# Performance work log

Hardware: AMD Instinct MI355X
Metric: run time of the kernel (lower is better)

Reference implementation:

```python
import jax, jax.numpy as jnp
import numpy as np

B, F, L, H, D = 8, 256, 1024, 4, 256   # batch, filters, seq_len, n_head(=dilation), d_qkv
MODEL = H * F                          # = H * D = 1024
WIN = 128                              # local_window_size


def _local_mask():
    m = np.ones((L, L), dtype=bool)
    m = np.tril(m, WIN - 1)
    m = np.triu(m, -(WIN - 1))
    return jnp.asarray(m)


def setup_inputs() -> dict:
    key = jax.random.key(0)
    ks = jax.random.split(key, 12)
    s = lambda n: 1.0 / np.sqrt(n)
    xav = np.sqrt(6.0 / (L + L))
    return {
        "x": jax.random.normal(ks[0], (B, F, L, H), jnp.float32),
        "Wq_w": jax.random.normal(ks[1], (D, F), jnp.float32) * s(F),
        "Wq_b": jnp.zeros((D,), jnp.float32),
        "Wk_w": jax.random.normal(ks[2], (D, F), jnp.float32) * s(F),
        "Wk_b": jnp.zeros((D,), jnp.float32),
        "Wv_w": jax.random.normal(ks[3], (D, F), jnp.float32) * s(F),
        "Wv_b": jnp.zeros((D,), jnp.float32),
        "w_bias": jax.random.uniform(ks[4], (L, L), jnp.float32, -xav, xav),
        "out_w": jax.random.normal(ks[5], (H * D, MODEL), jnp.float32) * s(H * D),
        "out_b": jnp.zeros((MODEL,), jnp.float32),
        "ln_g": jnp.ones((MODEL,), jnp.float32),
        "ln_b": jnp.zeros((MODEL,), jnp.float32),
        "local_mask": _local_mask(),
    }


def _flatten(y):
    # N C L H -> N L (H C): H outer, C inner in the flattened dim
    n = y.shape[0]
    return y.transpose(0, 2, 3, 1).reshape(n, L, -1)


def reference(x, Wq_w, Wq_b, Wk_w, Wk_b, Wv_w, Wv_b, w_bias, out_w, out_b, ln_g, ln_b, local_mask):
    def proj(w, b):
        # 1x1 Conv2d over (L,H) == channel matmul
        y = jnp.einsum('nclh,dc->ndlh', x, w) + b[None, :, None, None]
        return _flatten(y)

    q = proj(Wq_w, Wq_b)   # [B, L, H*D]
    k = proj(Wk_w, Wk_b)
    v = proj(Wv_w, Wv_b)

    wb = w_bias * local_mask.astype(w_bias.dtype)  # masked bias (masked entries -> 0, exp -> 1)
    ew = jnp.exp(wb)                                # [L, L]
    ek = jnp.exp(k)                                 # [B, L, H*D]
    num = jnp.einsum('ts,nsd->ntd', ew, ek * v)
    den = jnp.einsum('ts,nsd->ntd', ew, ek)
    y = jax.nn.sigmoid(q) * num / den               # [B, L, H*D]

    h = y @ out_w + out_b + _flatten(x)             # residual with flattened input
    mu = jnp.mean(h, axis=-1, keepdims=True)
    var = jnp.mean(jnp.square(h - mu), axis=-1, keepdims=True)
    return (h - mu) * jax.lax.rsqrt(var + 1e-5) * ln_g + ln_b
```

## Files before the change

### kernel.cpp

```cpp
#include <hip/hip_runtime.h>


typedef __attribute__((ext_vector_type(8))) short short8;
typedef __attribute__((ext_vector_type(4))) float f32x4;

#define MBYTE 1048576L

__device__ __forceinline__ unsigned short f2bf(float f) {
  unsigned u = __float_as_uint(f);
  unsigned r = (u + 0x7fff + ((u >> 16) & 1)) >> 16;
  return (unsigned short)r;
}
__device__ __forceinline__ float bf2f(unsigned short s) {
  return __uint_as_float(((unsigned)s) << 16);
}

__global__ void prep_weights(const float* __restrict__ Wq, const float* __restrict__ bq,
                             const float* __restrict__ Wk, const float* __restrict__ bk,
                             const float* __restrict__ Wv, const float* __restrict__ bv,
                             unsigned short* __restrict__ Btp, float* __restrict__ biascat) {
  int i = blockIdx.x * 256 + threadIdx.x;
  int r = i >> 8, c = i & 255;
  const float* W = (r < 256) ? Wq : ((r < 512) ? Wk : Wv);
  int rr = r & 255;
  Btp[i] = f2bf(W[rr * 256 + c]);
  if (c == 0) {
    const float* bp = (r < 256) ? bq : ((r < 512) ? bk : bv);
    biascat[r] = bp[rr];
  }
}

__global__ void prep_ew(const float* __restrict__ wbias, unsigned short* __restrict__ ew) {
  int i = blockIdx.x * 256 + threadIdx.x;
  int t = i >> 10, s = i & 1023;
  int d = t - s;
  float wb = (d >= -127 && d <= 127) ? wbias[i] : 0.0f;
  ew[i] = f2bf(__expf(wb));
}

__global__ void prep_outwT(const float* __restrict__ outw, unsigned short* __restrict__ outwT) {
  __shared__ float tle[32][33];
  int j0 = blockIdx.y * 32, m0 = blockIdx.x * 32;
  int tx = threadIdx.x;
  for (int r = threadIdx.y; r < 32; r += 8)
    tle[r][tx] = outw[(long)(j0 + r) * 1024 + m0 + tx];
  __syncthreads();
  for (int r = threadIdx.y; r < 32; r += 8)
    outwT[(long)(m0 + r) * 1024 + j0 + tx] = f2bf(tle[tx][r]);
}

__global__ void transpose_x(const float* __restrict__ x, unsigned short* __restrict__ xT) {
  __shared__ float tle[32][33];
  int n = blockIdx.z;
  int c0 = blockIdx.y * 32, lh0 = blockIdx.x * 32;
  int tx = threadIdx.x;
  for (int r = threadIdx.y; r < 32; r += 8)
    tle[r][tx] = x[(long)n * 1048576 + (long)(c0 + r) * 4096 + lh0 + tx];
  __syncthreads();
  for (int r = threadIdx.y; r < 32; r += 8) {
    int lh = lh0 + r, c = c0 + tx;
    int l = lh >> 2, h = lh & 3;
    xT[(long)n * 1048576 + (long)l * 1024 + h * 256 + c] = f2bf(tle[tx][r]);
  }
}

__global__ void transpose_ekv(const unsigned short* __restrict__ ekF,
                              const unsigned short* __restrict__ vF,
                              unsigned short* __restrict__ ekkT) {
  __shared__ unsigned short tEK[32][33];
  __shared__ unsigned short tEKV[32][33];
  int n = blockIdx.z;
  int l0 = blockIdx.y * 32, j0 = blockIdx.x * 32;
  int tx = threadIdx.x;
  for (int r = threadIdx.y; r < 32; r += 8) {
    long idx = (long)n * 1048576 + (long)(l0 + r) * 1024 + j0 + tx;
    unsigned short e = ekF[idx];
    unsigned short v = vF[idx];
    tEK[r][tx] = e;
    tEKV[r][tx] = f2bf(bf2f(e) * bf2f(v));
  }
  __syncthreads();
  for (int r = threadIdx.y; r < 32; r += 8) {
    int j = j0 + r, l = l0 + tx;
    ekkT[(long)n * 2097152 + (long)j * 1024 + l] = tEK[tx][r];
    ekkT[(long)n * 2097152 + (long)(1024 + j) * 1024 + l] = tEKV[tx][r];
  }
}

template <int EPI>
__global__ __launch_bounds__(256, 2) void gemm_bf16(
    const unsigned short* __restrict__ A, const unsigned short* __restrict__ Bt,
    int K, int lda, int ldb, long aBatch, long bBatch,
    const float* __restrict__ biascat,
    unsigned short* __restrict__ sq, unsigned short* __restrict__ ekF,
    unsigned short* __restrict__ vF,
    unsigned short* __restrict__ denB, unsigned short* __restrict__ numB,
    const float* __restrict__ outb, const float* __restrict__ xg,
    float* __restrict__ hbuf) {
  __shared__ unsigned short As[128 * 64];
  __shared__ unsigned short Bs[128 * 64];
  const int z = blockIdx.z;
  const unsigned short* Ab = A + (long)z * aBatch;
  const unsigned short* Bb = Bt + (long)z * bBatch;
  const int m0 = blockIdx.y * 128, n0 = blockIdx.x * 128;
  const int t = threadIdx.x, lane = t & 63;
  const int wrow = ((t >> 6) >> 1) * 64, wcol = ((t >> 6) & 1) * 64;

  f32x4 zero = {0.f, 0.f, 0.f, 0.f};
  f32x4 acc[4][4];
#pragma unroll
  for (int a = 0; a < 4; a++)
#pragma unroll
    for (int b = 0; b < 4; b++) acc[a][b] = zero;

  const int nK = K >> 6;
  for (int kt = 0; kt < nK; ++kt) {
    const int k0 = kt << 6;
#pragma unroll
    for (int i = 0; i < 4; i++) {
      const int e = (t + i * 256) * 8;
      const int r = e >> 6, kc = e & 63;
      __builtin_amdgcn_global_load_lds(
          (const __attribute__((address_space(1))) void*)(Ab + (long)(m0 + r) * lda + k0 + kc),
          (__attribute__((address_space(3))) void*)(As + e), 16, 0, 0);
    }
#pragma unroll
    for (int i = 0; i < 4; i++) {
      const int e = (t + i * 256) * 8;
      const int r = e >> 6, kc = e & 63;
      __builtin_amdgcn_global_load_lds(
          (const __attribute__((address_space(1))) void*)(Bb + (long)(n0 + r) * ldb + k0 + kc),
          (__attribute__((address_space(3))) void*)(Bs + e), 16, 0, 0);
    }
    __syncthreads();
#pragma unroll
    for (int ks = 0; ks < 2; ++ks) {
      short8 af[4], bfv[4];
      const int kk = ks * 32 + (lane >> 4) * 8;
#pragma unroll
      for (int fm = 0; fm < 4; fm++)
        af[fm] = *(const short8*)&As[(wrow + fm * 16 + (lane & 15)) * 64 + kk];
#pragma unroll
      for (int fn = 0; fn < 4; fn++)
        bfv[fn] = *(const short8*)&Bs[(wcol + fn * 16 + (lane & 15)) * 64 + kk];
#pragma unroll
      for (int fm = 0; fm < 4; fm++)
#pragma unroll
        for (int fn = 0; fn < 4; fn++)
          acc[fm][fn] =
              __builtin_amdgcn_mfma_f32_16x16x32_bf16(af[fm], bfv[fn], acc[fm][fn], 0, 0, 0);
    }
    __syncthreads();
  }

#pragma unroll
  for (int fm = 0; fm < 4; fm++) {
#pragma unroll
    for (int fn = 0; fn < 4; fn++) {
#pragma unroll
      for (int j = 0; j < 4; j++) {
        const int row = m0 + wrow + fm * 16 + ((lane >> 4) * 4 + j);
        const int col = n0 + wcol + fn * 16 + (lane & 15);
        float val = acc[fm][fn][j];
        if constexpr (EPI == 1) {
          val += biascat[col];
          const int n = row >> 12, l = (row >> 2) & 1023, h = row & 3;
          const long base = (long)n * 1048576 + (long)l * 1024 + h * 256;
          if (col < 256)
            sq[base + col] = f2bf(1.0f / (1.0f + __expf(-val)));
          else if (col < 512)
            ekF[base + (col - 256)] = f2bf(__expf(val));
          else
            vF[base + (col - 512)] = f2bf(val);
        } else if constexpr (EPI == 2) {
          const long base = (long)z * 1048576 + (long)row * 1024;
          if (col < 1024)
            denB[base + col] = f2bf(val);
          else
            numB[base + (col - 1024)] = f2bf(val);
        } else {
          const int n = row >> 10, l = row & 1023;
          const int h = col >> 8, c = col & 255;
          const long idx = (long)row * 1024 + col;
          hbuf[idx] = val + outb[col] + xg[(long)n * 1048576 + (long)c * 4096 + l * 4 + h];
        }
      }
    }
  }
}

__global__ void combine_y(const unsigned short* __restrict__ sq,
                          const unsigned short* __restrict__ denB,
                          const unsigned short* __restrict__ numB,
                          unsigned short* __restrict__ y) {
  const long i = (long)(blockIdx.x * 256 + threadIdx.x) * 4;
  ushort4 s = *(const ushort4*)(sq + i);
  ushort4 d = *(const ushort4*)(denB + i);
  ushort4 nu = *(const ushort4*)(numB + i);
  ushort4 r;
  r.x = f2bf(bf2f(s.x) * bf2f(nu.x) / bf2f(d.x));
  r.y = f2bf(bf2f(s.y) * bf2f(nu.y) / bf2f(d.y));
  r.z = f2bf(bf2f(s.z) * bf2f(nu.z) / bf2f(d.z));
  r.w = f2bf(bf2f(s.w) * bf2f(nu.w) / bf2f(d.w));
  *(ushort4*)(y + i) = r;
}

__global__ __launch_bounds__(256) void ln_k(const float* __restrict__ hbuf,
                                            const float* __restrict__ g,
                                            const float* __restrict__ bb,
                                            float* __restrict__ out) {
  __shared__ float red[16];
  const int row = blockIdx.x, t = threadIdx.x;
  const float4 hv = *(const float4*)(hbuf + (long)row * 1024 + t * 4);
  float s = hv.x + hv.y + hv.z + hv.w;
  float ss = hv.x * hv.x + hv.y * hv.y + hv.z * hv.z + hv.w * hv.w;
#pragma unroll
  for (int off = 32; off > 0; off >>= 1) {
    s += __shfl_down(s, off, 64);
    ss += __shfl_down(ss, off, 64);
  }
  const int wid = t >> 6;
  if ((t & 63) == 0) {
    red[wid] = s;
    red[8 + wid] = ss;
  }
  __syncthreads();
  const float tot = red[0] + red[1] + red[2] + red[3];
  const float tss = red[8] + red[9] + red[10] + red[11];
  const float mu = tot * (1.0f / 1024.0f);
  const float var = tss * (1.0f / 1024.0f) - mu * mu;
  const float rs = rsqrtf(var + 1e-5f);
  const float4 gv = *(const float4*)(g + t * 4);
  const float4 bv = *(const float4*)(bb + t * 4);
  float4 o;
  o.x = (hv.x - mu) * rs * gv.x + bv.x;
  o.y = (hv.y - mu) * rs * gv.y + bv.y;
  o.z = (hv.z - mu) * rs * gv.z + bv.z;
  o.w = (hv.w - mu) * rs * gv.w + bv.w;
  *(float4*)(out + (long)row * 1024 + t * 4) = o;
}

extern "C" void kernel_launch(void* const* d_in, const int* in_sizes, int n_in,
                              void* d_out, int out_size, void* d_ws, size_t ws_size,
                              hipStream_t stream) {
  (void)in_sizes; (void)n_in; (void)out_size; (void)ws_size;
  const float* x     = (const float*)d_in[0];
  const float* Wq_w  = (const float*)d_in[1];
  const float* Wq_b  = (const float*)d_in[2];
  const float* Wk_w  = (const float*)d_in[3];
  const float* Wk_b  = (const float*)d_in[4];
  const float* Wv_w  = (const float*)d_in[5];
  const float* Wv_b  = (const float*)d_in[6];
  const float* wbias = (const float*)d_in[7];
  const float* outw  = (const float*)d_in[8];
  const float* outb  = (const float*)d_in[9];
  const float* lng   = (const float*)d_in[10];
  const float* lnb   = (const float*)d_in[11];
  float* out = (float*)d_out;
  char* ws = (char*)d_ws;

  unsigned short* sq   = (unsigned short*)(ws + 0 * MBYTE);
  unsigned short* ekF  = (unsigned short*)(ws + 16 * MBYTE);
  unsigned short* vF   = (unsigned short*)(ws + 32 * MBYTE);
  unsigned short* xT   = (unsigned short*)(ws + 48 * MBYTE);
  unsigned short* ekkT = (unsigned short*)(ws + 48 * MBYTE);
  unsigned short* denB = (unsigned short*)(ws + 80 * MBYTE);
  unsigned short* numB = (unsigned short*)(ws + 96 * MBYTE);
  unsigned short* Btp  = (unsigned short*)(ws + 112 * MBYTE);
  float* biascat       = (float*)(ws + 112 * MBYTE + 393216);
  unsigned short* outwT= (unsigned short*)(ws + 112 * MBYTE + 397312);
  unsigned short* ew   = (unsigned short*)(ws + 112 * MBYTE + 397312 + 2097152);
  unsigned short* y    = ekF;
  float* hbuf          = (float*)(ws + 80 * MBYTE);

  prep_weights<<<768, 256, 0, stream>>>(Wq_w, Wq_b, Wk_w, Wk_b, Wv_w, Wv_b, Btp, biascat);
  prep_ew<<<4096, 256, 0, stream>>>(wbias, ew);
  prep_outwT<<<dim3(32, 32), dim3(32, 8), 0, stream>>>(outw, outwT);
  transpose_x<<<dim3(128, 8, 8), dim3(32, 8), 0, stream>>>(x, xT);

  gemm_bf16<1><<<dim3(6, 256, 1), 256, 0, stream>>>(
      xT, Btp, 256, 256, 256, 0L, 0L,
      biascat, sq, ekF, vF, nullptr, nullptr, nullptr, nullptr, nullptr);

  transpose_ekv<<<dim3(32, 32, 8), dim3(32, 8), 0, stream>>>(ekF, vF, ekkT);

  gemm_bf16<2><<<dim3(16, 8, 8), 256, 0, stream>>>(
      ew, ekkT, 1024, 1024, 1024, 0L, 2097152L,
      nullptr, nullptr, nullptr, nullptr, denB, numB, nullptr, nullptr, nullptr);

  combine_y<<<8192, 256, 0, stream>>>(sq, denB, numB, y);

  gemm_bf16<3><<<dim3(8, 64, 1), 256, 0, stream>>>(
      y, outwT, 1024, 1024, 1024, 0L, 0L,
      nullptr, nullptr, nullptr, nullptr, nullptr, nullptr, outb, x, hbuf);

  ln_k<<<8192, 256, 0, stream>>>(hbuf, lng, lnb, out);
}
```

Baseline: 288.2 us.

## Exploit banded mask via expm1 decomposition and column sums in attention GEMM

Rewrites exp(masked bias) as 1 + expm1(bias·mask). The all-ones part becomes per-batch column sums of ek and ek*v, accumulated with atomics in the transpose kernel and added in the GEMM epilogue. Because expm1 is zero outside the band, the num/den GEMM now loops only over K tiles that overlap the 128-wide window, skipping most of the 1024-long reduction. It also reads the residual from the already-transposed bf16 x instead of strided fp32 x. Risks include bf16 precision loss when adding large column sums, plus a new zeroing kernel and atomic traffic.

```diff
diff --git a/kernel.cpp b/kernel.cpp
--- a/kernel.cpp
+++ b/kernel.cpp
@@ -30,12 +30,12 @@
   }
 }
 
-__global__ void prep_ew(const float* __restrict__ wbias, unsigned short* __restrict__ ew) {
+__global__ void prep_ewm1(const float* __restrict__ wbias, unsigned short* __restrict__ ewm1) {
   int i = blockIdx.x * 256 + threadIdx.x;
   int t = i >> 10, s = i & 1023;
   int d = t - s;
-  float wb = (d >= -127 && d <= 127) ? wbias[i] : 0.0f;
-  ew[i] = f2bf(__expf(wb));
+  float v = (d >= -127 && d <= 127) ? expm1f(wbias[i]) : 0.0f;
+  ewm1[i] = f2bf(v);
 }
 
 __global__ void prep_outwT(const float* __restrict__ outw, unsigned short* __restrict__ outwT) {
@@ -47,6 +47,10 @@
   __syncthreads();
   for (int r = threadIdx.y; r < 32; r += 8)
     outwT[(long)(m0 + r) * 1024 + j0 + tx] = f2bf(tle[tx][r]);
+}
+
+__global__ void zero_S(float* __restrict__ S) {
+  S[blockIdx.x * 256 + threadIdx.x] = 0.0f;
 }
 
 __global__ void transpose_x(const float* __restrict__ x, unsigned short* __restrict__ xT) {
@@ -66,13 +70,15 @@
 
 __global__ void transpose_ekv(const unsigned short* __restrict__ ekF,
                               const unsigned short* __restrict__ vF,
-                              unsigned short* __restrict__ ekkT) {
+                              unsigned short* __restrict__ ekkT,
+                              float* __restrict__ S) {
   __shared__ unsigned short tEK[32][33];
   __shared__ unsigned short tEKV[32][33];
+  __shared__ float red[2][8][32];
   int n = blockIdx.z;
   int l0 = blockIdx.y * 32, j0 = blockIdx.x * 32;
-  int tx = threadIdx.x;
-  for (int r = threadIdx.y; r < 32; r += 8) {
+  int tx = threadIdx.x, ty = threadIdx.y;
+  for (int r = ty; r < 32; r += 8) {
     long idx = (long)n * 1048576 + (long)(l0 + r) * 1024 + j0 + tx;
     unsigned short e = ekF[idx];
     unsigned short v = vF[idx];
@@ -80,10 +86,29 @@
     tEKV[r][tx] = f2bf(bf2f(e) * bf2f(v));
   }
   __syncthreads();
-  for (int r = threadIdx.y; r < 32; r += 8) {
+  for (int r = ty; r < 32; r += 8) {
     int j = j0 + r, l = l0 + tx;
     ekkT[(long)n * 2097152 + (long)j * 1024 + l] = tEK[tx][r];
     ekkT[(long)n * 2097152 + (long)(1024 + j) * 1024 + l] = tEKV[tx][r];
+  }
+  float p0 = 0.f, p1 = 0.f;
+#pragma unroll
+  for (int q = 0; q < 4; q++) {
+    p0 += bf2f(tEK[ty + q * 8][tx]);
+    p1 += bf2f(tEKV[ty + q * 8][tx]);
+  }
+  red[0][ty][tx] = p0;
+  red[1][ty][tx] = p1;
+  __syncthreads();
+  if (ty == 0) {
+    float s0 = 0.f, s1 = 0.f;
+#pragma unroll
+    for (int q = 0; q < 8; q++) {
+      s0 += red[0][q][tx];
+      s1 += red[1][q][tx];
+    }
+    atomicAdd(&S[n * 2048 + j0 + tx], s0);
+    atomicAdd(&S[n * 2048 + 1024 + j0 + tx], s1);
   }
 }
 
@@ -95,7 +120,8 @@
     unsigned short* __restrict__ sq, unsigned short* __restrict__ ekF,
     unsigned short* __restrict__ vF,
     unsigned short* __restrict__ denB, unsigned short* __restrict__ numB,
-    const float* __restrict__ outb, const float* __restrict__ xg,
+    const float* __restrict__ Ssum,
+    const float* __restrict__ outb, const unsigned short* __restrict__ xTr,
     float* __restrict__ hbuf) {
   __shared__ unsigned short As[128 * 64];
   __shared__ unsigned short Bs[128 * 64];
@@ -113,8 +139,14 @@
 #pragma unroll
     for (int b = 0; b < 4; b++) acc[a][b] = zero;
 
-  const int nK = K >> 6;
-  for (int kt = 0; kt < nK; ++kt) {
+  int ktLo = 0, ktHi = (K >> 6) - 1;
+  if constexpr (EPI == 2) {
+    int sLo = m0 - 127; if (sLo < 0) sLo = 0;
+    int sHi = m0 + 254; if (sHi > 1023) sHi = 1023;
+    ktLo = sLo >> 6;
+    ktHi = sHi >> 6;
+  }
+  for (int kt = ktLo; kt <= ktHi; ++kt) {
     const int k0 = kt << 6;
 #pragma unroll
     for (int i = 0; i < 4; i++) {
@@ -173,16 +205,15 @@
           else
             vF[base + (col - 512)] = f2bf(val);
         } else if constexpr (EPI == 2) {
+          val += Ssum[z * 2048 + col];
           const long base = (long)z * 1048576 + (long)row * 1024;
           if (col < 1024)
             denB[base + col] = f2bf(val);
           else
             numB[base + (col - 1024)] = f2bf(val);
         } else {
-          const int n = row >> 10, l = row & 1023;
-          const int h = col >> 8, c = col & 255;
           const long idx = (long)row * 1024 + col;
-          hbuf[idx] = val + outb[col] + xg[(long)n * 1048576 + (long)c * 4096 + l * 4 + h];
+          hbuf[idx] = val + outb[col] + bf2f(xTr[idx]);
         }
       }
     }
@@ -261,38 +292,40 @@
 
   unsigned short* sq   = (unsigned short*)(ws + 0 * MBYTE);
   unsigned short* ekF  = (unsigned short*)(ws + 16 * MBYTE);
+  unsigned short* denB = (unsigned short*)(ws + 16 * MBYTE);
   unsigned short* vF   = (unsigned short*)(ws + 32 * MBYTE);
+  unsigned short* numB = (unsigned short*)(ws + 32 * MBYTE);
   unsigned short* xT   = (unsigned short*)(ws + 48 * MBYTE);
-  unsigned short* ekkT = (unsigned short*)(ws + 48 * MBYTE);
-  unsigned short* denB = (unsigned short*)(ws + 80 * MBYTE);
-  unsigned short* numB = (unsigned short*)(ws + 96 * MBYTE);
+  unsigned short* ekkT = (unsigned short*)(ws + 64 * MBYTE);
+  float* hbuf          = (float*)(ws + 64 * MBYTE);
+  unsigned short* y    = (unsigned short*)(ws + 96 * MBYTE);
   unsigned short* Btp  = (unsigned short*)(ws + 112 * MBYTE);
   float* biascat       = (float*)(ws + 112 * MBYTE + 393216);
   unsigned short* outwT= (unsigned short*)(ws + 112 * MBYTE + 397312);
-  unsigned short* ew   = (unsigned short*)(ws + 112 * MBYTE + 397312 + 2097152);
-  unsigned short* y    = ekF;
-  float* hbuf          = (float*)(ws + 80 * MBYTE);
+  unsigned short* ewm1 = (unsigned short*)(ws + 112 * MBYTE + 397312 + 2097152);
+  float* Ssum          = (float*)(ws + 112 * MBYTE + 397312 + 2 * 2097152);
 
   prep_weights<<<768, 256, 0, stream>>>(Wq_w, Wq_b, Wk_w, Wk_b, Wv_w, Wv_b, Btp, biascat);
-  prep_ew<<<4096, 256, 0, stream>>>(wbias, ew);
+  prep_ewm1<<<4096, 256, 0, stream>>>(wbias, ewm1);
   prep_outwT<<<dim3(32, 32), dim3(32, 8), 0, stream>>>(outw, outwT);
+  zero_S<<<64, 256, 0, stream>>>(Ssum);
   transpose_x<<<dim3(128, 8, 8), dim3(32, 8), 0, stream>>>(x, xT);
 
   gemm_bf16<1><<<dim3(6, 256, 1), 256, 0, stream>>>(
       xT, Btp, 256, 256, 256, 0L, 0L,
-      biascat, sq, ekF, vF, nullptr, nullptr, nullptr, nullptr, nullptr);
-
-  transpose_ekv<<<dim3(32, 32, 8), dim3(32, 8), 0, stream>>>(ekF, vF, ekkT);
+      biascat, sq, ekF, vF, nullptr, nullptr, nullptr, nullptr, nullptr, nullptr);
+
+  transpose_ekv<<<dim3(32, 32, 8), dim3(32, 8), 0, stream>>>(ekF, vF, ekkT, Ssum);
 
   gemm_bf16<2><<<dim3(16, 8, 8), 256, 0, stream>>>(
-      ew, ekkT, 1024, 1024, 1024, 0L, 2097152L,
-      nullptr, nullptr, nullptr, nullptr, denB, numB, nullptr, nullptr, nullptr);
+      ewm1, ekkT, 1024, 1024, 1024, 0L, 2097152L,
+      nullptr, nullptr, nullptr, nullptr, denB, numB, Ssum, nullptr, nullptr, nullptr);
 
   combine_y<<<8192, 256, 0, stream>>>(sq, denB, numB, y);
 
   gemm_bf16<3><<<dim3(8, 64, 1), 256, 0, stream>>>(
       y, outwT, 1024, 1024, 1024, 0L, 0L,
-      nullptr, nullptr, nullptr, nullptr, nullptr, nullptr, outb, x, hbuf);
+      nullptr, nullptr, nullptr, nullptr, nullptr, nullptr, nullptr, outb, xT, hbuf);
 
   ln_k<<<8192, 256, 0, stream>>>(hbuf, lng, lnb, out);
 }
```

Measured after the change: 251.6 us. -12.7%, faster.
